# Kernel tuning notes

Measured on AMD Instinct MI355X. Metric: run time of the kernel, lower is better.

Reference implementation:

```python
import jax, jax.numpy as jnp
import numpy as np

DIM = 384
HEADS = 6
HEAD_DIM = DIM // HEADS
HIDDEN = int(DIM * 4.0)
SCALE = HEAD_DIM ** (-0.5)
EPS = 1e-5


def _layernorm(x, w, b):
    m = jnp.mean(x, axis=-1, keepdims=True)
    v = jnp.var(x, axis=-1, keepdims=True)
    return (x - m) * jax.lax.rsqrt(v + EPS) * w + b


def _mlp(x, fc1_w, fc1_b, fc2_w, fc2_b):
    h = jnp.einsum('bnc,hc->bnh', x, fc1_w) + fc1_b
    h = jax.nn.gelu(h, approximate=False)  # torch nn.GELU default = exact erf
    return jnp.einsum('bnh,ch->bnc', h, fc2_w) + fc2_b


def _attn_block(q, k, v, proj_w, proj_b):
    # q:[B,H,Q,D] k,v:[B,H,K,D]
    attn = jnp.einsum('bhqd,bhkd->bhqk', q, k) * SCALE
    attn = jax.nn.softmax(attn, axis=-1)
    o = jnp.einsum('bhqk,bhkd->bhqd', attn, v)
    B, H, Q, D = o.shape
    o = o.transpose(0, 2, 1, 3).reshape(B, Q, H * D)
    return jnp.einsum('bqc,oc->bqo', o, proj_w) + proj_b


def setup_inputs() -> dict:
    key = jax.random.key(0)
    ks = jax.random.split(key, 10)
    s = 0.02
    return {
        'x': jax.random.normal(ks[0], (4, 2048, DIM), jnp.float32),
        'y': jax.random.normal(ks[1], (4, 256, DIM), jnp.float32),
        'norm1_w': jnp.ones((DIM,), jnp.float32),
        'norm1_b': jnp.zeros((DIM,), jnp.float32),
        'norm2_w': jnp.ones((DIM,), jnp.float32),
        'norm2_b': jnp.zeros((DIM,), jnp.float32),
        'qkv_w': jax.random.normal(ks[2], (3 * DIM, DIM), jnp.float32) * s,
        'proj_w': jax.random.normal(ks[3], (DIM, DIM), jnp.float32) * s,
        'proj_b': jnp.zeros((DIM,), jnp.float32),
        'fc1_w': jax.random.normal(ks[4], (HIDDEN, DIM), jnp.float32) * s,
        'fc1_b': jnp.zeros((HIDDEN,), jnp.float32),
        'fc2_w': jax.random.normal(ks[5], (DIM, HIDDEN), jnp.float32) * s,
        'fc2_b': jnp.zeros((DIM,), jnp.float32),
    }


def reference(x, y, norm1_w, norm1_b, norm2_w, norm2_b, qkv_w,
              proj_w, proj_b, fc1_w, fc1_b, fc2_w, fc2_b):
    B, N, C = x.shape
    L = y.shape[1]
    nx = _layernorm(x, norm1_w, norm1_b)
    ny = _layernorm(y, norm1_w, norm1_b)
    cat = jnp.concatenate([nx, ny], axis=1)  # [B, N+L, C]
    qkv = jnp.einsum('bnc,oc->bno', cat, qkv_w)
    qkv = qkv.reshape(B, N + L, 3, HEADS, HEAD_DIM).transpose(2, 0, 3, 1, 4)
    q, k, v = qkv[0], qkv[1], qkv[2]  # each [B,H,N+L,D]
    # cross: y-queries attend over all N+L keys
    y_att = _attn_block(q[:, :, N:], k, v, proj_w, proj_b)
    # self: x-queries attend over first N keys only
    x_att = _attn_block(q[:, :, :N], k[:, :, :N], v[:, :, :N], proj_w, proj_b)
    new_x = x + x_att
    new_y = y + y_att
    new_x = new_x + _mlp(_layernorm(new_x, norm2_w, norm2_b), fc1_w, fc1_b, fc2_w, fc2_b)
    new_y = new_y + _mlp(_layernorm(new_y, norm2_w, norm2_b), fc1_w, fc1_b, fc2_w, fc2_b)
    return (new_x, new_y)
```

## Files before the change

### kernel.cpp

```cpp
#include <hip/hip_runtime.h>
#include <hip/hip_bf16.h>
#include <math.h>

#define B_   4
#define NX   2048
#define NY   256
#define T_   2304
#define NTOK 9216
#define DIM  384
#define NH   6
#define HD   64
#define HID  1536
#define QKV3 1152
#define QK2  768

typedef __attribute__((ext_vector_type(8))) short bf16x8;
typedef __attribute__((ext_vector_type(4))) float f32x4;

__device__ __forceinline__ float b2f(unsigned short u) {
  union { unsigned int i; float f; } x; x.i = ((unsigned int)u) << 16; return x.f;
}
__device__ __forceinline__ unsigned short f2b(float f) {
  union { float f; unsigned int i; } x; x.f = f;
  unsigned int r = x.i + 0x7fffu + ((x.i >> 16) & 1u);
  return (unsigned short)(r >> 16);
}
__device__ __forceinline__ unsigned int pack2(float a, float b) {
  return (unsigned int)f2b(a) | ((unsigned int)f2b(b) << 16);
}
__device__ __forceinline__ unsigned int cvtpk(float a, float b) {
  unsigned int r;
  asm("v_cvt_pk_bf16_f32 %0, %1, %2" : "=v"(r) : "v"(a), "v"(b));
  return r;
}
__device__ __forceinline__ float fexp2(float x) {
  float r;
  asm("v_exp_f32 %0, %1" : "=v"(r) : "v"(x));
  return r;
}
__device__ __forceinline__ float ldin(const void* p, size_t i, int isbf) {
  return isbf ? b2f(((const unsigned short*)p)[i]) : ((const float*)p)[i];
}

#if defined(__has_builtin)
#if __has_builtin(__builtin_amdgcn_global_load_lds)
#define HAS_GLL 1
#endif
#endif

__device__ __forceinline__ void stage16(const unsigned short* g, unsigned short* l) {
#ifdef HAS_GLL
  __builtin_amdgcn_global_load_lds(
      (const __attribute__((address_space(1))) unsigned int*)g,
      (__attribute__((address_space(3))) unsigned int*)l, 16, 0, 0);
#else
  *(uint4*)(l + (threadIdx.x & 63) * 8) = *(const uint4*)g;
#endif
}

__global__ void detect_kernel(const unsigned short* __restrict__ qw,
                              int* __restrict__ flag) {
  int lane = threadIdx.x;
  int bad = 0;
  #pragma unroll
  for (int j = 0; j < 8; j++) {
    unsigned short u = qw[2 * (lane + 64 * j)];
    int e = (u >> 7) & 0xff;
    bad += (e >= 134) ? 1 : 0;
  }
  #pragma unroll
  for (int off = 32; off > 0; off >>= 1) bad += __shfl_xor(bad, off);
  if (lane == 0) *flag = (bad < 64) ? 1 : 0;
}

__global__ __launch_bounds__(256) void convert4_kernel(
    const void* __restrict__ s0, const void* __restrict__ s1,
    const void* __restrict__ s2, const void* __restrict__ s3,
    unsigned short* __restrict__ d0, const int* __restrict__ flagp) {
  int isbf = *flagp;
  int i = (blockIdx.x * 256 + threadIdx.x) * 8;
  const void* src; int off, K_;
  if (i < 442368)       { src = s0; off = 0;       K_ = 384;  }
  else if (i < 589824)  { src = s1; off = 442368;  K_ = 384;  }
  else if (i < 1179648) { src = s2; off = 589824;  K_ = 384;  }
  else                  { src = s3; off = 1179648; K_ = 1536; }
  int li = i - off;
  int rts = 64 * K_;
  int tn = li / rts, rem = li - tn * rts;
  int tk = rem >> 11, q = rem & 2047;
  int w = q >> 9, l = (q >> 3) & 63;
  int row = tn * 64 + w * 16 + (l >> 2);
  int col = tk * 32 + (((l & 3) ^ ((l >> 3) & 3)) << 3);
  size_t s = (size_t)row * K_ + col;
  if (isbf) {
    *(uint4*)(d0 + i) = *(const uint4*)((const unsigned short*)src + s);
  } else {
    const float* sp = (const float*)src + s;
    unsigned int wv[4];
    #pragma unroll
    for (int j = 0; j < 4; j++) wv[j] = pack2(sp[2 * j], sp[2 * j + 1]);
    *(uint4*)(d0 + i) = make_uint4(wv[0], wv[1], wv[2], wv[3]);
  }
}

__global__ __launch_bounds__(256) void ln1_kernel(
    const void* __restrict__ x, const void* __restrict__ y,
    const void* __restrict__ w, const void* __restrict__ bsh,
    const int* __restrict__ flagp, unsigned short* __restrict__ out)
{
  int isbf = *flagp;
  int token = blockIdx.x * 4 + (threadIdx.x >> 6);
  int lane  = threadIdx.x & 63;
  int bb = token / T_;
  int t  = token - bb * T_;
  const void* src = (t < NX) ? x : y;
  size_t base = (t < NX) ? ((size_t)bb * NX + t) * DIM
                         : ((size_t)bb * NY + (t - NX)) * DIM;
  float v[6];
  float s = 0.f, s2 = 0.f;
  #pragma unroll
  for (int k = 0; k < 6; k++) {
    v[k] = ldin(src, base + lane + 64 * k, isbf);
    s += v[k]; s2 += v[k] * v[k];
  }
  #pragma unroll
  for (int off = 32; off > 0; off >>= 1) {
    s  += __shfl_xor(s, off);
    s2 += __shfl_xor(s2, off);
  }
  float mean = s * (1.f / DIM);
  float var  = s2 * (1.f / DIM) - mean * mean;
  float rs = rsqrtf(var + 1e-5f);
  unsigned short* dst = out + (size_t)token * DIM;
  #pragma unroll
  for (int k = 0; k < 6; k++) {
    int c = lane + 64 * k;
    dst[c] = f2b((v[k] - mean) * rs * ldin(w, c, isbf) + ldin(bsh, c, isbf));
  }
}

__global__ __launch_bounds__(256) void ln2_kernel(
    const float* __restrict__ in, const void* __restrict__ w,
    const void* __restrict__ bsh, const int* __restrict__ flagp,
    unsigned short* __restrict__ out)
{
  int isbf = *flagp;
  int token = blockIdx.x * 4 + (threadIdx.x >> 6);
  int lane  = threadIdx.x & 63;
  const float* src = in + (size_t)token * DIM;
  float v[6];
  float s = 0.f, s2 = 0.f;
  #pragma unroll
  for (int k = 0; k < 6; k++) {
    v[k] = src[lane + 64 * k];
    s += v[k]; s2 += v[k] * v[k];
  }
  #pragma unroll
  for (int off = 32; off > 0; off >>= 1) {
    s  += __shfl_xor(s, off);
    s2 += __shfl_xor(s2, off);
  }
  float mean = s * (1.f / DIM);
  float var  = s2 * (1.f / DIM) - mean * mean;
  float rs = rsqrtf(var + 1e-5f);
  unsigned short* dst = out + (size_t)token * DIM;
  #pragma unroll
  for (int k = 0; k < 6; k++) {
    int c = lane + 64 * k;
    dst[c] = f2b((v[k] - mean) * rs * ldin(w, c, isbf) + ldin(bsh, c, isbf));
  }
}

template <int EPI, int KT, int MT>
__global__ __launch_bounds__(256, (MT == 64) ? 6 : 4) void gemm_mfma(
    const unsigned short* __restrict__ A, const unsigned short* __restrict__ Bw,
    const void* __restrict__ bias,
    const void* __restrict__ rx, const void* __restrict__ ry,
    const float* __restrict__ rf,
    unsigned short* __restrict__ outb, float* __restrict__ resf,
    void* __restrict__ outd, unsigned short* __restrict__ vTp,
    const int* __restrict__ flagp, int N)
{
  constexpr int NT = KT / 32;
  constexpr int NI = MT / 64;
  __shared__ unsigned short As[2][MT * 32];
  __shared__ unsigned short Bs[2][64 * 32];
  const int tid  = threadIdx.x;
  const int wave = tid >> 6, lane = tid & 63;
  const int g = lane >> 4, qq = lane & 15;
  const int gx = gridDim.x;
  const int flat = blockIdx.x + gx * blockIdx.y;
  const int cpx = (gx * gridDim.y) >> 3;
  const int L = (flat & 7) * cpx + (flat >> 3);
  const int n0 = (L % gx) * 64, m0 = (L / gx) * MT;
  const int wm = wave * (16 * NI);

  f32x4 z = {0.f, 0.f, 0.f, 0.f};
  f32x4 acc[NI][4];
  #pragma unroll
  for (int i = 0; i < NI; i++)
    #pragma unroll
    for (int j = 0; j < 4; j++) acc[i][j] = z;

  const int lrow = lane >> 2;
  const int lkx  = (((lane & 3) ^ ((lane >> 3) & 3)) * 8);
  const int rsw  = (qq >> 1) & 3;

  const unsigned short* Bbase = Bw + (size_t)(n0 >> 6) * NT * 2048 +
                                wave * 512 + lane * 8;

  auto STG = [&](int t, int bi_) {
    int k0_ = t * 32;
    #pragma unroll
    for (int s = 0; s < NI; s++) {
      int ar = wm + s * 16;
      stage16(A + (size_t)(m0 + ar + lrow) * KT + k0_ + lkx,
              &As[bi_][ar * 32]);
    }
    stage16(Bbase + (size_t)t * 2048, &Bs[bi_][wave * 16 * 32]);
  };
  auto COMPUTE = [&](int bi_) {
    const unsigned short* as = As[bi_];
    const unsigned short* bs = Bs[bi_];
    bf16x8 af[NI], bf[4];
    #pragma unroll
    for (int i = 0; i < NI; i++)
      af[i] = *(const bf16x8*)&as[(wm + i * 16 + qq) * 32 + ((g ^ rsw) * 8)];
    #pragma unroll
    for (int j = 0; j < 4; j++)
      bf[j] = *(const bf16x8*)&bs[(j * 16 + qq) * 32 + ((g ^ rsw) * 8)];
    __builtin_amdgcn_s_setprio(1);
    #pragma unroll
    for (int i = 0; i < NI; i++)
      #pragma unroll
      for (int j = 0; j < 4; j++)
        acc[i][j] = __builtin_amdgcn_mfma_f32_16x16x32_bf16(
            af[i], bf[j], acc[i][j], 0, 0, 0);
    __builtin_amdgcn_s_setprio(0);
  };
  #define GSYNC() do { \
    asm volatile("s_waitcnt vmcnt(0)" ::: "memory"); \
    __builtin_amdgcn_s_barrier(); } while (0)

  STG(0, 0);
  GSYNC();
  #pragma unroll 1
  for (int t = 0; t + 2 < NT; t += 2) {
    STG(t + 1, 1);
    COMPUTE(0);
    GSYNC();
    STG(t + 2, 0);
    COMPUTE(1);
    GSYNC();
  }
  STG(NT - 1, 1);
  COMPUTE(0);
  GSYNC();
  COMPUTE(1);
  #undef GSYNC

  if (EPI == 0 && n0 >= 768) {
    #pragma unroll
    for (int i = 0; i < NI; i++) {
      int mb = m0 + wm + i * 16 + g * 4;
      int bb = mb / T_;
      int t  = mb - bb * T_;
      #pragma unroll
      for (int j = 0; j < 4; j++) {
        int n = n0 + j * 16 + qq;
        int hh = (n - 768) >> 6, dd = (n - 768) & 63;
        uint2 pk;
        pk.x = pack2(acc[i][j][0], acc[i][j][1]);
        pk.y = pack2(acc[i][j][2], acc[i][j][3]);
        *(uint2*)(vTp + ((size_t)(bb * NH + hh) * HD + dd) * T_ + t) = pk;
      }
    }
    return;
  }

  int isbf = (EPI == 0) ? 1 : *flagp;
  float qs = (EPI == 0 && n0 < 384) ? 0.18033688011f : 1.f;
  const bool kswz = (EPI == 0) && (n0 >= 384);
  #pragma unroll
  for (int i = 0; i < NI; i++) {
    #pragma unroll
    for (int r = 0; r < 4; r++) {
      int m = m0 + wm + i * 16 + g * 4 + r;
      int bb = m / T_;
      int t  = m - bb * T_;
      int l = m & 31;
      int ms = kswz ? ((m & ~31) | (((l >> 2) & 1) << 4) | ((l >> 3) << 2) |
                       (l & 3))
                    : m;
      #pragma unroll
      for (int j = 0; j < 4; j++) {
        int n = n0 + j * 16 + qq;
        float v = acc[i][j][r];
        if (EPI == 0) {
          outb[(size_t)ms * QK2 + n] = f2b(v * qs);
        } else if (EPI == 1) {
          float resv = (t < NX)
              ? ldin(rx, ((size_t)bb * NX + t) * DIM + n, isbf)
              : ldin(ry, ((size_t)bb * NY + (t - NX)) * DIM + n, isbf);
          resf[(size_t)m * DIM + n] = v + ldin(bias, n, isbf) + resv;
        } else if (EPI == 2) {
          float h = v + ldin(bias, n, isbf);
          outb[(size_t)m * N + n] =
              f2b(0.5f * h * (1.f + erff(h * 0.70710678118654752f)));
        } else {
          float rr = v + ldin(bias, n, isbf) + rf[(size_t)m * DIM + n];
          size_t oi = (t < NX)
              ? ((size_t)bb * NX + t) * DIM + n
              : (size_t)B_ * NX * DIM + ((size_t)bb * NY + (t - NX)) * DIM + n;
          if (isbf) ((unsigned short*)outd)[oi] = f2b(rr);
          else      ((float*)outd)[oi] = rr;
        }
      }
    }
  }
}

__global__ __launch_bounds__(256) void attn_mfma(
    const unsigned short* __restrict__ qk, const unsigned short* __restrict__ vT,
    unsigned short* __restrict__ att)
{
  __shared__ float Ob[64][68];
  __shared__ float Lb[64];
  const int tid = threadIdx.x;
  const int wave = tid >> 6, lane = tid & 63;
  const int g = lane >> 4, qq = lane & 15;
  const int flat = blockIdx.x;
  const int L = (flat & 7) * 108 + (flat >> 3);
  const int bx = L % 36;
  const int hb = L / 36;
  const int h = hb % NH, b = hb / NH;
  const int self = (bx < 32);
  const int qtok0 = self ? bx * 64 : NX + (bx - 32) * 64;
  const int kvbeg = wave * (self ? 512 : 576);
  const int ntile = self ? 16 : 18;

  bf16x8 qa[4][2];
  #pragma unroll
  for (int f = 0; f < 4; f++) {
    size_t qrow = (size_t)(b * T_ + qtok0 + f * 16 + qq) * QK2 + h * HD;
    qa[f][0] = *(const bf16x8*)(qk + qrow + g * 8);
    qa[f][1] = *(const bf16x8*)(qk + qrow + 32 + g * 8);
  }
  const unsigned short* kb = qk + (size_t)b * T_ * QK2 + DIM + h * HD;
  const unsigned short* vb = vT + (size_t)(b * NH + h) * HD * T_;

  f32x4 z = {0.f, 0.f, 0.f, 0.f};
  f32x4 ot[4][4];
  #pragma unroll
  for (int f = 0; f < 4; f++)
    #pragma unroll
    for (int dt = 0; dt < 4; dt++) ot[f][dt] = z;
  float lsum[4] = {0.f, 0.f, 0.f, 0.f};

  const unsigned short* kp0 = kb + (size_t)(kvbeg + qq) * QK2 + g * 8;
  const unsigned short* kp1 = kp0 + 16 * QK2;
  const unsigned short* vp0 = vb + (size_t)qq * T_ + kvbeg + g * 8;
  const unsigned short* vp1 = vp0 + 16 * T_;
  const unsigned short* vp2 = vp0 + 32 * T_;
  const unsigned short* vp3 = vp0 + 48 * T_;

  uint4 kc[4];
  kc[0] = *(const uint4*)(kp0);
  kc[1] = *(const uint4*)(kp0 + 32);
  kc[2] = *(const uint4*)(kp1);
  kc[3] = *(const uint4*)(kp1 + 32);
  kp0 += 32 * QK2; kp1 += 32 * QK2;
  uint4 vc[4];
  vc[0] = *(const uint4*)(vp0);
  vc[1] = *(const uint4*)(vp1);
  vc[2] = *(const uint4*)(vp2);
  vc[3] = *(const uint4*)(vp3);
  vp0 += 32; vp1 += 32; vp2 += 32; vp3 += 32;

  for (int it = 0; it < ntile; it++) {
    f32x4 s[4][2];
    __builtin_amdgcn_s_setprio(1);
    #pragma unroll
    for (int f = 0; f < 4; f++) {
      s[f][0] = __builtin_amdgcn_mfma_f32_16x16x32_bf16(
          *(const bf16x8*)&kc[0], qa[f][0], z, 0, 0, 0);
      s[f][0] = __builtin_amdgcn_mfma_f32_16x16x32_bf16(
          *(const bf16x8*)&kc[1], qa[f][1], s[f][0], 0, 0, 0);
      s[f][1] = __builtin_amdgcn_mfma_f32_16x16x32_bf16(
          *(const bf16x8*)&kc[2], qa[f][0], z, 0, 0, 0);
      s[f][1] = __builtin_amdgcn_mfma_f32_16x16x32_bf16(
          *(const bf16x8*)&kc[3], qa[f][1], s[f][1], 0, 0, 0);
    }
    __builtin_amdgcn_s_setprio(0);
    if (it + 1 < ntile) {
      kc[0] = *(const uint4*)(kp0);
      kc[1] = *(const uint4*)(kp0 + 32);
      kc[2] = *(const uint4*)(kp1);
      kc[3] = *(const uint4*)(kp1 + 32);
      kp0 += 32 * QK2; kp1 += 32 * QK2;
    }

    #pragma unroll
    for (int f = 0; f < 4; f++) {
      float pv[8];
      #pragma unroll
      for (int c = 0; c < 2; c++)
        #pragma unroll
        for (int r = 0; r < 4; r++)
          pv[c * 4 + r] = fexp2(s[f][c][r]);
      lsum[f] += ((pv[0] + pv[1]) + (pv[2] + pv[3])) +
                 ((pv[4] + pv[5]) + (pv[6] + pv[7]));
      union { unsigned int w[4]; bf16x8 v; } bq;
      bq.w[0] = cvtpk(pv[0], pv[1]);
      bq.w[1] = cvtpk(pv[2], pv[3]);
      bq.w[2] = cvtpk(pv[4], pv[5]);
      bq.w[3] = cvtpk(pv[6], pv[7]);
      __builtin_amdgcn_s_setprio(1);
      #pragma unroll
      for (int dt = 0; dt < 4; dt++)
        ot[f][dt] = __builtin_amdgcn_mfma_f32_16x16x32_bf16(
            *(const bf16x8*)&vc[dt], bq.v, ot[f][dt], 0, 0, 0);
      __builtin_amdgcn_s_setprio(0);
    }

    if (it + 1 < ntile) {
      vc[0] = *(const uint4*)(vp0);
      vc[1] = *(const uint4*)(vp1);
      vc[2] = *(const uint4*)(vp2);
      vc[3] = *(const uint4*)(vp3);
      vp0 += 32; vp1 += 32; vp2 += 32; vp3 += 32;
    }
  }

  #pragma unroll
  for (int f = 0; f < 4; f++) {
    lsum[f] += __shfl_xor(lsum[f], 16);
    lsum[f] += __shfl_xor(lsum[f], 32);
  }

  #pragma unroll
  for (int w = 0; w < 4; w++) {
    if (wave == w) {
      if (w == 0) {
        #pragma unroll
        for (int f = 0; f < 4; f++) {
          #pragma unroll
          for (int dt = 0; dt < 4; dt++)
            *(f32x4*)&Ob[f * 16 + qq][dt * 16 + g * 4] = ot[f][dt];
          if (g == 0) Lb[f * 16 + qq] = lsum[f];
        }
      } else {
        #pragma unroll
        for (int f = 0; f < 4; f++) {
          #pragma unroll
          for (int dt = 0; dt < 4; dt++) {
            f32x4 cur = *(const f32x4*)&Ob[f * 16 + qq][dt * 16 + g * 4];
            #pragma unroll
            for (int r = 0; r < 4; r++) cur[r] += ot[f][dt][r];
            *(f32x4*)&Ob[f * 16 + qq][dt * 16 + g * 4] = cur;
          }
          if (g == 0) Lb[f * 16 + qq] += lsum[f];
        }
      }
    }
    __syncthreads();
  }

  int q = tid >> 2, ds = (tid & 3) * 16;
  float inv = 1.f / Lb[q];
  float o[16];
  #pragma unroll
  for (int j = 0; j < 16; j += 4) {
    f32x4 a = *(const f32x4*)&Ob[q][ds + j];
    #pragma unroll
    for (int r = 0; r < 4; r++) o[j + r] = a[r] * inv;
  }
  unsigned int w[8];
  #pragma unroll
  for (int j = 0; j < 8; j++) w[j] = pack2(o[2 * j], o[2 * j + 1]);
  size_t orow = (size_t)(b * T_ + qtok0 + q) * DIM + h * HD + ds;
  *(uint4*)(att + orow)     = make_uint4(w[0], w[1], w[2], w[3]);
  *(uint4*)(att + orow + 8) = make_uint4(w[4], w[5], w[6], w[7]);
}

extern "C" void kernel_launch(void* const* d_in, const int* in_sizes, int n_in,
                              void* d_out, int out_size, void* d_ws, size_t ws_size,
                              hipStream_t stream)
{
  (void)in_sizes; (void)n_in; (void)out_size; (void)ws_size;
  const void* x    = d_in[0];
  const void* y    = d_in[1];
  const void* n1w  = d_in[2];
  const void* n1b  = d_in[3];
  const void* n2w  = d_in[4];
  const void* n2b  = d_in[5];
  const void* qkvw = d_in[6];
  const void* pw   = d_in[7];
  const void* pb   = d_in[8];
  const void* f1w  = d_in[9];
  const void* f1b  = d_in[10];
  const void* f2w  = d_in[11];
  const void* f2bp = d_in[12];

  unsigned short* wsu = (unsigned short*)d_ws;
  int* flag = (int*)d_ws;
  unsigned short* wts    = wsu + 128;
  unsigned short* qkvw_b = wts;
  unsigned short* pw_b   = wts + 442368;
  unsigned short* f1w_b  = wts + 589824;
  unsigned short* f2w_b  = wts + 1179648;
  unsigned short* catln  = wsu + 1769600;
  unsigned short* qkvb2  = wsu + 5308544;
  unsigned short* attb   = wsu + 12386432;
  unsigned short* vT     = wsu + 15925376;
  unsigned short* hbuf   = qkvb2;
  float*          resb   = (float*)d_ws + 9732160;

  detect_kernel<<<1, 64, 0, stream>>>((const unsigned short*)qkvw, flag);
  convert4_kernel<<<864, 256, 0, stream>>>(qkvw, pw, f1w, f2w, wts, flag);

  ln1_kernel<<<NTOK / 4, 256, 0, stream>>>(x, y, n1w, n1b, flag, catln);
  gemm_mfma<0, DIM, 128><<<dim3(QKV3 / 64, NTOK / 128), 256, 0, stream>>>(
      catln, qkvw_b, nullptr, nullptr, nullptr, nullptr, qkvb2, nullptr,
      nullptr, vT, flag, QKV3);
  attn_mfma<<<dim3(864), 256, 0, stream>>>(qkvb2, vT, attb);
  gemm_mfma<1, DIM, 64><<<dim3(DIM / 64, NTOK / 64), 256, 0, stream>>>(
      attb, pw_b, pb, x, y, nullptr, nullptr, resb, nullptr, nullptr,
      flag, DIM);
  ln2_kernel<<<NTOK / 4, 256, 0, stream>>>(resb, n2w, n2b, flag, catln);
  gemm_mfma<2, DIM, 128><<<dim3(HID / 64, NTOK / 128), 256, 0, stream>>>(
      catln, f1w_b, f1b, nullptr, nullptr, nullptr, hbuf, nullptr, nullptr,
      nullptr, flag, HID);
  gemm_mfma<3, HID, 64><<<dim3(DIM / 64, NTOK / 64), 256, 0, stream>>>(
      hbuf, f2w_b, f2bp, nullptr, nullptr, resb, nullptr, nullptr, d_out,
      nullptr, flag, DIM);
}
```

Baseline: 271.7 us.

## Store GEMM A-operand activations in pre-tiled swizzled layout for contiguous staging

Producers of GEMM A operands (layernorm kernels, attention output, GELU epilogue) now write bf16 activations in a packed tile layout that matches the LDS swizzle, mirroring how weights are already packed. The GEMM A staging then becomes one contiguous 16-byte-per-lane load per 16-row chunk instead of strided row gathers. This is meant to cut address computation and make global-to-LDS loads fully coalesced. In exchange the producer stores become scattered per element (layernorm, GELU), which may cost coalescing on the write side.

```diff
diff --git a/kernel.cpp b/kernel.cpp
--- a/kernel.cpp
+++ b/kernel.cpp
@@ -40,6 +40,13 @@
 }
 __device__ __forceinline__ float ldin(const void* p, size_t i, int isbf) {
   return isbf ? b2f(((const unsigned short*)p)[i]) : ((const float*)p)[i];
+}
+
+__device__ __forceinline__ size_t pkidx(int m, int c, int ntk) {
+  int r4 = m & 15;
+  int j = ((c >> 3) & 3) ^ ((r4 >> 1) & 3);
+  return ((size_t)((m >> 6) * ntk + (c >> 5))) * 2048 +
+         (size_t)(((m >> 4) & 3) * 512 + (r4 * 4 + j) * 8 + (c & 7));
 }
 
 #if defined(__has_builtin)
@@ -131,11 +138,11 @@
   float mean = s * (1.f / DIM);
   float var  = s2 * (1.f / DIM) - mean * mean;
   float rs = rsqrtf(var + 1e-5f);
-  unsigned short* dst = out + (size_t)token * DIM;
   #pragma unroll
   for (int k = 0; k < 6; k++) {
     int c = lane + 64 * k;
-    dst[c] = f2b((v[k] - mean) * rs * ldin(w, c, isbf) + ldin(bsh, c, isbf));
+    out[pkidx(token, c, 12)] =
+        f2b((v[k] - mean) * rs * ldin(w, c, isbf) + ldin(bsh, c, isbf));
   }
 }
 
@@ -163,11 +170,11 @@
   float mean = s * (1.f / DIM);
   float var  = s2 * (1.f / DIM) - mean * mean;
   float rs = rsqrtf(var + 1e-5f);
-  unsigned short* dst = out + (size_t)token * DIM;
   #pragma unroll
   for (int k = 0; k < 6; k++) {
     int c = lane + 64 * k;
-    dst[c] = f2b((v[k] - mean) * rs * ldin(w, c, isbf) + ldin(bsh, c, isbf));
+    out[pkidx(token, c, 12)] =
+        f2b((v[k] - mean) * rs * ldin(w, c, isbf) + ldin(bsh, c, isbf));
   }
 }
 
@@ -202,22 +209,23 @@
     #pragma unroll
     for (int j = 0; j < 4; j++) acc[i][j] = z;
 
-  const int lrow = lane >> 2;
-  const int lkx  = (((lane & 3) ^ ((lane >> 3) & 3)) * 8);
   const int rsw  = (qq >> 1) & 3;
 
   const unsigned short* Bbase = Bw + (size_t)(n0 >> 6) * NT * 2048 +
                                 wave * 512 + lane * 8;
+  const unsigned short* Abase[NI];
+  #pragma unroll
+  for (int s = 0; s < NI; s++) {
+    int ci = wave * NI + s;
+    Abase[s] = A + (size_t)((m0 >> 6) + (ci >> 2)) * NT * 2048 +
+               (ci & 3) * 512 + lane * 8;
+  }
 
   auto STG = [&](int t, int bi_) {
-    int k0_ = t * 32;
-    #pragma unroll
-    for (int s = 0; s < NI; s++) {
-      int ar = wm + s * 16;
-      stage16(A + (size_t)(m0 + ar + lrow) * KT + k0_ + lkx,
-              &As[bi_][ar * 32]);
-    }
-    stage16(Bbase + (size_t)t * 2048, &Bs[bi_][wave * 16 * 32]);
+    #pragma unroll
+    for (int s = 0; s < NI; s++)
+      stage16(Abase[s] + (size_t)t * 2048, &As[bi_][(wm + s * 16) * 32]);
+    stage16(Bbase + (size_t)t * 2048, &Bs[bi_][wave * 512]);
   };
   auto COMPUTE = [&](int bi_) {
     const unsigned short* as = As[bi_];
@@ -305,7 +313,7 @@
           resf[(size_t)m * DIM + n] = v + ldin(bias, n, isbf) + resv;
         } else if (EPI == 2) {
           float h = v + ldin(bias, n, isbf);
-          outb[(size_t)m * N + n] =
+          outb[pkidx(m, n, 48)] =
               f2b(0.5f * h * (1.f + erff(h * 0.70710678118654752f)));
         } else {
           float rr = v + ldin(bias, n, isbf) + rf[(size_t)m * DIM + n];
@@ -478,9 +486,10 @@
   unsigned int w[8];
   #pragma unroll
   for (int j = 0; j < 8; j++) w[j] = pack2(o[2 * j], o[2 * j + 1]);
-  size_t orow = (size_t)(b * T_ + qtok0 + q) * DIM + h * HD + ds;
-  *(uint4*)(att + orow)     = make_uint4(w[0], w[1], w[2], w[3]);
-  *(uint4*)(att + orow + 8) = make_uint4(w[4], w[5], w[6], w[7]);
+  int mt = b * T_ + qtok0 + q;
+  int c0 = h * HD + ds;
+  *(uint4*)(att + pkidx(mt, c0, 12))     = make_uint4(w[0], w[1], w[2], w[3]);
+  *(uint4*)(att + pkidx(mt, c0 + 8, 12)) = make_uint4(w[4], w[5], w[6], w[7]);
 }
 
 extern "C" void kernel_launch(void* const* d_in, const int* in_sizes, int n_in,
```

Measured after the change: 268.2 us. Within noise of the previous version (-1.3%).
